# Performance work log

Measured on AMD Instinct MI355X. Metric: run time of the kernel, lower is better.

The kernel has to match this reference:

```python
import jax, jax.numpy as jnp
import numpy as np

NUM_HEADS = 12
MASK_BIAS = -1000.0


def setup_inputs() -> dict:
    key = jax.random.key(0)
    k1, k2, k3, k4 = jax.random.split(key, 4)
    B, N, C = 2, 2048, 768
    x = jax.random.normal(k1, (B, N, C), dtype=jnp.float32)
    # key-padding mask: 1.0 = masked-out position (gets -1000 bias), 0.0 = visible
    mask = jax.random.randint(k2, (B, N), 0, 2).astype(jnp.float32)
    qkv_w = jax.random.normal(k3, (3 * C, C), dtype=jnp.float32) * (1.0 / np.sqrt(C))
    proj_w = jax.random.normal(k4, (C, C), dtype=jnp.float32) * (1.0 / np.sqrt(C))
    proj_b = jnp.zeros((C,), dtype=jnp.float32)
    return {"x": x, "mask": mask, "qkv_w": qkv_w, "proj_w": proj_w, "proj_b": proj_b}


def reference(x, mask, qkv_w, proj_w, proj_b):
    B, N, C = x.shape
    H = NUM_HEADS
    D = C // H
    scale = D ** (-0.5)
    # qkv: Linear without bias -> [B, N, 3C] -> [3, B, H, N, D]
    qkv = (x @ qkv_w.T).reshape(B, N, 3, H, D).transpose(2, 0, 3, 1, 4)
    q, k, v = qkv[0], qkv[1], qkv[2]
    # scores [B, H, N, N]
    attn = jnp.einsum("bhqd,bhkd->bhqk", q, k) * scale
    attn = attn + mask[:, None, None, :] * MASK_BIAS
    attn = jax.nn.softmax(attn, axis=-1)
    out = jnp.einsum("bhqk,bhkd->bhqd", attn, v)  # [B, H, N, D]
    out = out.transpose(0, 2, 1, 3).reshape(B, N, C)
    return out @ proj_w.T + proj_b
```

## Files before the change

kernel.cpp:

```cpp
#include <hip/hip_runtime.h>

typedef __bf16 bf16_t;
typedef __bf16 bf16x8 __attribute__((ext_vector_type(8)));
typedef float f32x4 __attribute__((ext_vector_type(4)));

#define NUM_B 2
#define NUM_H 12
#define SEQ_N 2048
#define DIM_C 768
#define HEAD_D 64
#define BH_CNT (NUM_B * NUM_H)
#define MTOK (NUM_B * SEQ_N)
#define QSCALE 0.1803368801111137f

#define AS1(p) ((const __attribute__((address_space(1))) void*)(p))
#define AS3(p) ((__attribute__((address_space(3))) void*)(p))

__global__ __launch_bounds__(256) void cvt_scan_kernel(
    const float* __restrict__ s0, const float* __restrict__ s1,
    const float* __restrict__ s2, const float* __restrict__ msk,
    bf16_t* __restrict__ d0, bf16_t* __restrict__ d1, bf16_t* __restrict__ d2,
    int* __restrict__ src, bf16_t* __restrict__ wp, int* __restrict__ cnts,
    int nb0, int nb1, int nb2) {
  __shared__ int psum[256];
  const int blk = blockIdx.x;
  const int t = threadIdx.x;
  if (blk >= nb0 + nb1 + nb2) {
    const int b = blk - (nb0 + nb1 + nb2);
    const float* mb = msk + (size_t)b * SEQ_N;
    int vis[8], c = 0;
#pragma unroll
    for (int j = 0; j < 8; ++j) {
      vis[j] = (mb[t * 8 + j] == 0.0f) ? 1 : 0;
      c += vis[j];
    }
    psum[t] = c;
    __syncthreads();
    for (int off = 1; off < 256; off <<= 1) {
      int v = (t >= off) ? psum[t - off] : 0;
      __syncthreads();
      psum[t] += v;
      __syncthreads();
    }
    const int total = psum[255];
    int vpos = psum[t] - c;
    int mpos = total + (t * 8 - (psum[t] - c));
#pragma unroll
    for (int j = 0; j < 8; ++j) {
      const int tok = t * 8 + j;
      if (vis[j]) {
        src[b * SEQ_N + vpos] = b * SEQ_N + tok;
        wp[b * SEQ_N + vpos] = (bf16_t)1.0f;
        ++vpos;
      } else {
        src[b * SEQ_N + mpos] = b * SEQ_N + tok;
        wp[b * SEQ_N + mpos] = (bf16_t)0.0f;
        ++mpos;
      }
    }
    if (t == 0) {
      cnts[b * 2] = (total + 63) & ~63;
      cnts[b * 2 + 1] = total;
    }
    return;
  }
  const float* sp;
  bf16_t* dp;
  size_t off;
  if (blk < nb0) {
    sp = s0; dp = d0; off = (size_t)blk * 2048;
  } else if (blk < nb0 + nb1) {
    sp = s1; dp = d1; off = (size_t)(blk - nb0) * 2048;
  } else {
    sp = s2; dp = d2; off = (size_t)(blk - nb0 - nb1) * 2048;
  }
  const size_t i = off + (size_t)t * 8;
  float4 f0 = *reinterpret_cast<const float4*>(&sp[i]);
  float4 f1 = *reinterpret_cast<const float4*>(&sp[i + 4]);
  union { ushort4 u; bf16_t h[4]; } p0, p1;
  p0.h[0] = (bf16_t)f0.x; p0.h[1] = (bf16_t)f0.y;
  p0.h[2] = (bf16_t)f0.z; p0.h[3] = (bf16_t)f0.w;
  p1.h[0] = (bf16_t)f1.x; p1.h[1] = (bf16_t)f1.y;
  p1.h[2] = (bf16_t)f1.z; p1.h[3] = (bf16_t)f1.w;
  *reinterpret_cast<ushort4*>(&dp[i]) = p0.u;
  *reinterpret_cast<ushort4*>(&dp[i + 4]) = p1.u;
}

__global__ __launch_bounds__(256, 3) void gemm_qkv_kernel(
    const bf16_t* __restrict__ A, const bf16_t* __restrict__ W,
    const int* __restrict__ src, const int* __restrict__ cnts,
    bf16_t* __restrict__ out) {
  __shared__ __align__(16) bf16_t As[2][128 * 32];
  __shared__ __align__(16) bf16_t Bs[2][128 * 32];

  const int tid = threadIdx.x;
  const int wave = tid >> 6, lane = tid & 63;
  const int quad = lane >> 4, l16 = lane & 15;
  const int m0 = blockIdx.y * 128, n0 = blockIdx.x * 128;
  const int wm = (wave >> 1) * 64, wn = (wave & 1) * 64;
  const bool isQ = (n0 < DIM_C);

  if (!isQ) {
    const int b = m0 >> 11;
    if ((m0 & 2047) >= cnts[b * 2]) return;
  }

  f32x4 acc[4][4] = {};

  const int srow = tid >> 2;
  const int scol = ((tid & 3) ^ ((tid >> 3) & 3)) * 8;
  int ar0, ar1;
  if (isQ) {
    ar0 = m0 + srow;
    ar1 = m0 + srow + 64;
  } else {
    ar0 = src[m0 + srow];
    ar1 = src[m0 + srow + 64];
  }
  const bf16_t* gA0 = A + (size_t)ar0 * DIM_C + scol;
  const bf16_t* gA1 = A + (size_t)ar1 * DIM_C + scol;
  const bf16_t* gB0 = W + (size_t)(n0 + srow) * DIM_C + scol;
  const bf16_t* gB1 = W + (size_t)(n0 + srow + 64) * DIM_C + scol;
  const int lb = wave * 512;

  auto issue = [&](int buf, int k0) {
    __builtin_amdgcn_global_load_lds(AS1(gA0 + k0), AS3(&As[buf][lb]), 16, 0, 0);
    __builtin_amdgcn_global_load_lds(AS1(gA1 + k0), AS3(&As[buf][lb + 2048]), 16, 0, 0);
    __builtin_amdgcn_global_load_lds(AS1(gB0 + k0), AS3(&Bs[buf][lb]), 16, 0, 0);
    __builtin_amdgcn_global_load_lds(AS1(gB1 + k0), AS3(&Bs[buf][lb + 2048]), 16, 0, 0);
  };

  issue(0, 0);
  int cur = 0;
  const int sw = (l16 >> 1) & 3;
  for (int step = 0; step < DIM_C / 32; ++step) {
    __syncthreads();
    if (step + 1 < DIM_C / 32) issue(cur ^ 1, (step + 1) * 32);

    bf16x8 aF[4], bF[4];
#pragma unroll
    for (int mi = 0; mi < 4; ++mi)
      aF[mi] = *reinterpret_cast<const bf16x8*>(
          &As[cur][(wm + mi * 16 + l16) * 32 + ((quad ^ sw) * 8)]);
#pragma unroll
    for (int ni = 0; ni < 4; ++ni)
      bF[ni] = *reinterpret_cast<const bf16x8*>(
          &Bs[cur][(wn + ni * 16 + l16) * 32 + ((quad ^ sw) * 8)]);
#pragma unroll
    for (int mi = 0; mi < 4; ++mi)
#pragma unroll
      for (int ni = 0; ni < 4; ++ni)
        acc[mi][ni] = __builtin_amdgcn_mfma_f32_16x16x32_bf16(aF[mi], bF[ni],
                                                              acc[mi][ni], 0, 0, 0);
    cur ^= 1;
  }

  const size_t per = (size_t)BH_CNT * SEQ_N * HEAD_D;
#pragma unroll
  for (int mi = 0; mi < 4; ++mi) {
#pragma unroll
    for (int ni = 0; ni < 4; ++ni) {
      const int gmB = m0 + wm + mi * 16 + quad * 4;
      const int gn = n0 + wn + ni * 16 + l16;
      const int b = gmB >> 11;
      if (isQ) {
        const int h = gn >> 6, d = gn & 63;
#pragma unroll
        for (int r = 0; r < 4; ++r) {
          const int gm = gmB + r;
          const int tok = gm & 2047;
          out[(((size_t)((gm >> 11) * NUM_H + h) * SEQ_N + tok) * HEAD_D + d)] =
              (bf16_t)(acc[mi][ni][r] * QSCALE);
        }
      } else if (n0 < 2 * DIM_C) {
        const int rem = gn - DIM_C;
        const int h = rem >> 6, d = rem & 63;
#pragma unroll
        for (int r = 0; r < 4; ++r) {
          const int pos = (gmB + r) & 2047;
          out[per + (((size_t)(b * NUM_H + h) * SEQ_N + pos) * HEAD_D + d)] =
              (bf16_t)acc[mi][ni][r];
        }
      } else {
        const int rem = gn - 2 * DIM_C;
        const int h = rem >> 6, d = rem & 63;
        const int pos0 = gmB & 2047;
        const int count = cnts[b * 2 + 1];
        union { ushort4 u; bf16_t h4[4]; } pk;
#pragma unroll
        for (int r = 0; r < 4; ++r)
          pk.h4[r] = (pos0 + r < count) ? (bf16_t)acc[mi][ni][r] : (bf16_t)0.0f;
        *reinterpret_cast<ushort4*>(
            &out[2 * per + (((size_t)(b * NUM_H + h) * HEAD_D + d) * SEQ_N + pos0)]) =
            pk.u;
      }
    }
  }
}

__global__ __launch_bounds__(256, 3) void gemm_proj_kernel(
    const bf16_t* __restrict__ A, const bf16_t* __restrict__ W,
    const float* __restrict__ bias, float* __restrict__ out) {
  __shared__ __align__(16) bf16_t As[2][128 * 32];
  __shared__ __align__(16) bf16_t Bs[2][128 * 32];

  const int tid = threadIdx.x;
  const int wave = tid >> 6, lane = tid & 63;
  const int quad = lane >> 4, l16 = lane & 15;
  const int m0 = blockIdx.y * 128, n0 = blockIdx.x * 128;
  const int wm = (wave >> 1) * 64, wn = (wave & 1) * 64;

  f32x4 acc[4][4] = {};

  const int srow = tid >> 2;
  const int scol = ((tid & 3) ^ ((tid >> 3) & 3)) * 8;
  const bf16_t* gA0 = A + (size_t)(m0 + srow) * DIM_C + scol;
  const bf16_t* gA1 = A + (size_t)(m0 + srow + 64) * DIM_C + scol;
  const bf16_t* gB0 = W + (size_t)(n0 + srow) * DIM_C + scol;
  const bf16_t* gB1 = W + (size_t)(n0 + srow + 64) * DIM_C + scol;
  const int lb = wave * 512;

  auto issue = [&](int buf, int k0) {
    __builtin_amdgcn_global_load_lds(AS1(gA0 + k0), AS3(&As[buf][lb]), 16, 0, 0);
    __builtin_amdgcn_global_load_lds(AS1(gA1 + k0), AS3(&As[buf][lb + 2048]), 16, 0, 0);
    __builtin_amdgcn_global_load_lds(AS1(gB0 + k0), AS3(&Bs[buf][lb]), 16, 0, 0);
    __builtin_amdgcn_global_load_lds(AS1(gB1 + k0), AS3(&Bs[buf][lb + 2048]), 16, 0, 0);
  };

  issue(0, 0);
  int cur = 0;
  const int sw = (l16 >> 1) & 3;
  for (int step = 0; step < DIM_C / 32; ++step) {
    __syncthreads();
    if (step + 1 < DIM_C / 32) issue(cur ^ 1, (step + 1) * 32);

    bf16x8 aF[4], bF[4];
#pragma unroll
    for (int mi = 0; mi < 4; ++mi)
      aF[mi] = *reinterpret_cast<const bf16x8*>(
          &As[cur][(wm + mi * 16 + l16) * 32 + ((quad ^ sw) * 8)]);
#pragma unroll
    for (int ni = 0; ni < 4; ++ni)
      bF[ni] = *reinterpret_cast<const bf16x8*>(
          &Bs[cur][(wn + ni * 16 + l16) * 32 + ((quad ^ sw) * 8)]);
#pragma unroll
    for (int mi = 0; mi < 4; ++mi)
#pragma unroll
      for (int ni = 0; ni < 4; ++ni)
        acc[mi][ni] = __builtin_amdgcn_mfma_f32_16x16x32_bf16(aF[mi], bF[ni],
                                                              acc[mi][ni], 0, 0, 0);
    cur ^= 1;
  }

#pragma unroll
  for (int mi = 0; mi < 4; ++mi) {
#pragma unroll
    for (int ni = 0; ni < 4; ++ni) {
      const int gmB = m0 + wm + mi * 16 + quad * 4;
      const int gn = n0 + wn + ni * 16 + l16;
      const float bv = bias[gn];
#pragma unroll
      for (int r = 0; r < 4; ++r)
        out[(size_t)(gmB + r) * DIM_C + gn] = acc[mi][ni][r] + bv;
    }
  }
}

__global__ __launch_bounds__(256, 4) void attn_kernel(
    const bf16_t* __restrict__ q, const bf16_t* __restrict__ k,
    const bf16_t* __restrict__ vt, const bf16_t* __restrict__ wp,
    const int* __restrict__ cnts, bf16_t* __restrict__ ctx) {
  __shared__ __align__(16) bf16_t Ks[2][64 * 64];
  __shared__ __align__(16) bf16_t Vs[2][64 * 64];
  __shared__ __align__(16) bf16_t Ps[4][1024];

  const int tid = threadIdx.x;
  const int wave = tid >> 6, lane = tid & 63;
  const int quad = lane >> 4, l16 = lane & 15;
  const int bh = blockIdx.y;
  const int b = bh / NUM_H, h = bh - b * NUM_H;
  const int q0 = blockIdx.x * 64 + wave * 16;
  const int cntPad = cnts[b * 2];

  const bf16_t* qb = q + (size_t)bh * SEQ_N * HEAD_D;
  const bf16_t* kb = k + (size_t)bh * SEQ_N * HEAD_D;
  const bf16_t* vtb = vt + (size_t)bh * HEAD_D * SEQ_N;
  const bf16_t* wb = wp + (size_t)b * SEQ_N;

  bf16x8 qf[2];
#pragma unroll
  for (int ks = 0; ks < 2; ++ks)
    qf[ks] = *reinterpret_cast<const bf16x8*>(
        &qb[(size_t)(q0 + l16) * HEAD_D + ks * 32 + quad * 8]);

  f32x4 acc[4] = {};
  f32x4 acc_l = {};

  const int srow = tid >> 3;
  const int scol = ((tid & 7) ^ ((tid >> 3) & 7)) * 8;
  const bf16_t* gK0 = kb + (size_t)srow * HEAD_D + scol;
  const bf16_t* gK1 = kb + (size_t)(srow + 32) * HEAD_D + scol;
  const bf16_t* gV0 = vtb + (size_t)srow * SEQ_N + scol;
  const bf16_t* gV1 = vtb + (size_t)(srow + 32) * SEQ_N + scol;
  const int lb = wave * 512;

  auto issueKV = [&](int buf, int key0) {
    __builtin_amdgcn_global_load_lds(AS1(gK0 + (size_t)key0 * HEAD_D),
                                     AS3(&Ks[buf][lb]), 16, 0, 0);
    __builtin_amdgcn_global_load_lds(AS1(gK1 + (size_t)key0 * HEAD_D),
                                     AS3(&Ks[buf][lb + 2048]), 16, 0, 0);
    __builtin_amdgcn_global_load_lds(AS1(gV0 + key0), AS3(&Vs[buf][lb]), 16, 0, 0);
    __builtin_amdgcn_global_load_lds(AS1(gV1 + key0), AS3(&Vs[buf][lb + 2048]),
                                     16, 0, 0);
  };

  issueKV(0, 0);
  int cur = 0;
  const int swz = l16 & 7;
  const int psbase = wave * 1024 + l16 * 64;
  for (int key0 = 0; key0 < cntPad; key0 += 64) {
    __syncthreads();
    if (key0 + 64 < cntPad) issueKV(cur ^ 1, key0 + 64);

    f32x4 s[4];
#pragma unroll
    for (int kt = 0; kt < 4; ++kt) {
      const int row = kt * 16 + l16;
      bf16x8 kf0 = *reinterpret_cast<const bf16x8*>(
          &Ks[cur][row * 64 + ((quad ^ swz) * 8)]);
      bf16x8 kf1 = *reinterpret_cast<const bf16x8*>(
          &Ks[cur][row * 64 + (((4 + quad) ^ swz) * 8)]);
      f32x4 z = {0.0f, 0.0f, 0.0f, 0.0f};
      z = __builtin_amdgcn_mfma_f32_16x16x32_bf16(kf0, qf[0], z, 0, 0, 0);
      s[kt] = __builtin_amdgcn_mfma_f32_16x16x32_bf16(kf1, qf[1], z, 0, 0, 0);
    }

#pragma unroll
    for (int kt = 0; kt < 4; ++kt) {
      union { ushort4 u; bf16_t h4[4]; } pk;
      pk.h4[0] = (bf16_t)exp2f(s[kt][0]);
      pk.h4[1] = (bf16_t)exp2f(s[kt][1]);
      pk.h4[2] = (bf16_t)exp2f(s[kt][2]);
      pk.h4[3] = (bf16_t)exp2f(s[kt][3]);
      const int c = kt * 2 + (quad >> 1);
      *reinterpret_cast<ushort4*>(
          &Ps[0][psbase + ((c ^ swz) << 3) + ((quad & 1) << 2)]) = pk.u;
    }

    bf16x8 pf0 = *reinterpret_cast<const bf16x8*>(
        &Ps[0][psbase + ((quad ^ swz) << 3)]);
    bf16x8 pf1 = *reinterpret_cast<const bf16x8*>(
        &Ps[0][psbase + (((4 + quad) ^ swz) << 3)]);
    bf16x8 wf0 = *reinterpret_cast<const bf16x8*>(&wb[key0 + quad * 8]);
    bf16x8 wf1 = *reinterpret_cast<const bf16x8*>(&wb[key0 + 32 + quad * 8]);
    acc_l = __builtin_amdgcn_mfma_f32_16x16x32_bf16(pf0, wf0, acc_l, 0, 0, 0);
    acc_l = __builtin_amdgcn_mfma_f32_16x16x32_bf16(pf1, wf1, acc_l, 0, 0, 0);

#pragma unroll
    for (int dt = 0; dt < 4; ++dt) {
      const int row = dt * 16 + l16;
      bf16x8 vf0 = *reinterpret_cast<const bf16x8*>(
          &Vs[cur][row * 64 + ((quad ^ swz) * 8)]);
      bf16x8 vf1 = *reinterpret_cast<const bf16x8*>(
          &Vs[cur][row * 64 + (((4 + quad) ^ swz) * 8)]);
      acc[dt] = __builtin_amdgcn_mfma_f32_16x16x32_bf16(pf0, vf0, acc[dt], 0, 0, 0);
      acc[dt] = __builtin_amdgcn_mfma_f32_16x16x32_bf16(pf1, vf1, acc[dt], 0, 0, 0);
    }
    cur ^= 1;
  }

  float rl[4];
#pragma unroll
  for (int r = 0; r < 4; ++r) rl[r] = 1.0f / acc_l[r];
#pragma unroll
  for (int dt = 0; dt < 4; ++dt)
#pragma unroll
    for (int r = 0; r < 4; ++r) {
      const int tok = q0 + quad * 4 + r;
      ctx[((size_t)b * SEQ_N + tok) * DIM_C + h * HEAD_D + dt * 16 + l16] =
          (bf16_t)(acc[dt][r] * rl[r]);
    }
}

extern "C" void kernel_launch(void* const* d_in, const int* in_sizes, int n_in,
                              void* d_out, int out_size, void* d_ws,
                              size_t ws_size, hipStream_t stream) {
  const float* x = (const float*)d_in[0];
  const float* mask = (const float*)d_in[1];
  const float* qkv_w = (const float*)d_in[2];
  const float* proj_w = (const float*)d_in[3];
  const float* proj_b = (const float*)d_in[4];
  float* out = (float*)d_out;

  const size_t nx = (size_t)MTOK * DIM_C;
  const size_t nqw = (size_t)3 * DIM_C * DIM_C;
  const size_t npw = (size_t)DIM_C * DIM_C;
  const size_t per = (size_t)BH_CNT * SEQ_N * HEAD_D;

  bf16_t* xb = (bf16_t*)d_ws;
  bf16_t* qwb = xb + nx;
  bf16_t* pwb = qwb + nqw;
  bf16_t* wpb = pwb + npw;
  int* srcb = (int*)(wpb + MTOK);
  int* cntsb = srcb + MTOK;
  bf16_t* qkv = (bf16_t*)(cntsb + 8);
  bf16_t* ctx = qkv + 3 * per;

  const int nb0 = (int)(nx / 2048), nb1 = (int)(nqw / 2048),
            nb2 = (int)(npw / 2048);

  cvt_scan_kernel<<<nb0 + nb1 + nb2 + NUM_B, 256, 0, stream>>>(
      x, qkv_w, proj_w, mask, xb, qwb, pwb, srcb, wpb, cntsb, nb0, nb1, nb2);
  gemm_qkv_kernel<<<dim3(3 * DIM_C / 128, MTOK / 128), 256, 0, stream>>>(
      xb, qwb, srcb, cntsb, qkv);
  attn_kernel<<<dim3(SEQ_N / 64, BH_CNT), 256, 0, stream>>>(
      qkv, qkv + per, qkv + 2 * per, wpb, cntsb, ctx);
  gemm_proj_kernel<<<dim3(DIM_C / 128, MTOK / 128), 256, 0, stream>>>(
      ctx, pwb, proj_b, out);
}
```

Measured before the change: 150.5 us.

## Stage only K in LDS with 128-key tiles, read V directly from global

The attention loop now double-buffers only K in shared memory and uses 128-key tiles, split into two 64-key halves per barrier. V fragments are loaded straight from global memory into registers for each half. This halves the number of barriers and frees LDS that V staging used to occupy. In exchange, V loads are no longer prefetched through LDS and may expose global latency; the occupancy hint also drops from 4 to 3 blocks.

```diff
diff --git a/kernel.cpp b/kernel.cpp
--- a/kernel.cpp
+++ b/kernel.cpp
@@ -266,12 +266,11 @@
   }
 }
 
-__global__ __launch_bounds__(256, 4) void attn_kernel(
+__global__ __launch_bounds__(256, 3) void attn_kernel(
     const bf16_t* __restrict__ q, const bf16_t* __restrict__ k,
     const bf16_t* __restrict__ vt, const bf16_t* __restrict__ wp,
     const int* __restrict__ cnts, bf16_t* __restrict__ ctx) {
-  __shared__ __align__(16) bf16_t Ks[2][64 * 64];
-  __shared__ __align__(16) bf16_t Vs[2][64 * 64];
+  __shared__ __align__(16) bf16_t Ks[2][128 * 64];
   __shared__ __align__(16) bf16_t Ps[4][1024];
 
   const int tid = threadIdx.x;
@@ -297,74 +296,81 @@
   f32x4 acc_l = {};
 
   const int srow = tid >> 3;
-  const int scol = ((tid & 7) ^ ((tid >> 3) & 7)) * 8;
-  const bf16_t* gK0 = kb + (size_t)srow * HEAD_D + scol;
-  const bf16_t* gK1 = kb + (size_t)(srow + 32) * HEAD_D + scol;
-  const bf16_t* gV0 = vtb + (size_t)srow * SEQ_N + scol;
-  const bf16_t* gV1 = vtb + (size_t)(srow + 32) * SEQ_N + scol;
+  const int scol = ((tid & 7) ^ (srow & 7)) * 8;
+  const bf16_t* gK = kb + (size_t)srow * HEAD_D + scol;
   const int lb = wave * 512;
 
-  auto issueKV = [&](int buf, int key0) {
-    __builtin_amdgcn_global_load_lds(AS1(gK0 + (size_t)key0 * HEAD_D),
-                                     AS3(&Ks[buf][lb]), 16, 0, 0);
-    __builtin_amdgcn_global_load_lds(AS1(gK1 + (size_t)key0 * HEAD_D),
-                                     AS3(&Ks[buf][lb + 2048]), 16, 0, 0);
-    __builtin_amdgcn_global_load_lds(AS1(gV0 + key0), AS3(&Vs[buf][lb]), 16, 0, 0);
-    __builtin_amdgcn_global_load_lds(AS1(gV1 + key0), AS3(&Vs[buf][lb + 2048]),
-                                     16, 0, 0);
+  auto issueK = [&](int buf, int key0) {
+#pragma unroll
+    for (int p = 0; p < 4; ++p)
+      __builtin_amdgcn_global_load_lds(
+          AS1(gK + (size_t)(key0 + p * 32) * HEAD_D),
+          AS3(&Ks[buf][p * 2048 + lb]), 16, 0, 0);
   };
 
-  issueKV(0, 0);
+  issueK(0, 0);
   int cur = 0;
   const int swz = l16 & 7;
   const int psbase = wave * 1024 + l16 * 64;
-  for (int key0 = 0; key0 < cntPad; key0 += 64) {
+
+  for (int key0 = 0; key0 < cntPad; key0 += 128) {
     __syncthreads();
-    if (key0 + 64 < cntPad) issueKV(cur ^ 1, key0 + 64);
-
-    f32x4 s[4];
-#pragma unroll
-    for (int kt = 0; kt < 4; ++kt) {
-      const int row = kt * 16 + l16;
-      bf16x8 kf0 = *reinterpret_cast<const bf16x8*>(
-          &Ks[cur][row * 64 + ((quad ^ swz) * 8)]);
-      bf16x8 kf1 = *reinterpret_cast<const bf16x8*>(
-          &Ks[cur][row * 64 + (((4 + quad) ^ swz) * 8)]);
-      f32x4 z = {0.0f, 0.0f, 0.0f, 0.0f};
-      z = __builtin_amdgcn_mfma_f32_16x16x32_bf16(kf0, qf[0], z, 0, 0, 0);
-      s[kt] = __builtin_amdgcn_mfma_f32_16x16x32_bf16(kf1, qf[1], z, 0, 0, 0);
-    }
-
-#pragma unroll
-    for (int kt = 0; kt < 4; ++kt) {
-      union { ushort4 u; bf16_t h4[4]; } pk;
-      pk.h4[0] = (bf16_t)exp2f(s[kt][0]);
-      pk.h4[1] = (bf16_t)exp2f(s[kt][1]);
-      pk.h4[2] = (bf16_t)exp2f(s[kt][2]);
-      pk.h4[3] = (bf16_t)exp2f(s[kt][3]);
-      const int c = kt * 2 + (quad >> 1);
-      *reinterpret_cast<ushort4*>(
-          &Ps[0][psbase + ((c ^ swz) << 3) + ((quad & 1) << 2)]) = pk.u;
-    }
-
-    bf16x8 pf0 = *reinterpret_cast<const bf16x8*>(
-        &Ps[0][psbase + ((quad ^ swz) << 3)]);
-    bf16x8 pf1 = *reinterpret_cast<const bf16x8*>(
-        &Ps[0][psbase + (((4 + quad) ^ swz) << 3)]);
-    bf16x8 wf0 = *reinterpret_cast<const bf16x8*>(&wb[key0 + quad * 8]);
-    bf16x8 wf1 = *reinterpret_cast<const bf16x8*>(&wb[key0 + 32 + quad * 8]);
-    acc_l = __builtin_amdgcn_mfma_f32_16x16x32_bf16(pf0, wf0, acc_l, 0, 0, 0);
-    acc_l = __builtin_amdgcn_mfma_f32_16x16x32_bf16(pf1, wf1, acc_l, 0, 0, 0);
-
-#pragma unroll
-    for (int dt = 0; dt < 4; ++dt) {
-      const int row = dt * 16 + l16;
-      bf16x8 vf0 = *reinterpret_cast<const bf16x8*>(
-          &Vs[cur][row * 64 + ((quad ^ swz) * 8)]);
-      bf16x8 vf1 = *reinterpret_cast<const bf16x8*>(
-          &Vs[cur][row * 64 + (((4 + quad) ^ swz) * 8)]);
-      acc[dt] = __builtin_amdgcn_mfma_f32_16x16x32_bf16(pf0, vf0, acc[dt], 0, 0, 0);
-      acc[dt] = __builtin_amdgcn_mfma_f32_16x16x32_bf16(pf1, vf1, acc[dt], 0, 0, 0);
+    if (key0 + 128 < cntPad) issueK(cur ^ 1, key0 + 128);
+
+#pragma unroll
+    for (int hf = 0; hf < 2; ++hf) {
+      const int kbase = key0 + hf * 64;
+      if (kbase >= cntPad) break;
+
+      bf16x8 vf[4][2];
+#pragma unroll
+      for (int dt = 0; dt < 4; ++dt) {
+        const bf16_t* vr = &vtb[(size_t)(dt * 16 + l16) * SEQ_N + kbase];
+        vf[dt][0] = *reinterpret_cast<const bf16x8*>(&vr[quad * 8]);
+        vf[dt][1] = *reinterpret_cast<const bf16x8*>(&vr[32 + quad * 8]);
+      }
+
+      f32x4 s[4];
+#pragma unroll
+      for (int kt = 0; kt < 4; ++kt) {
+        const int row = hf * 64 + kt * 16 + l16;
+        bf16x8 kf0 = *reinterpret_cast<const bf16x8*>(
+            &Ks[cur][row * 64 + ((quad ^ swz) * 8)]);
+        bf16x8 kf1 = *reinterpret_cast<const bf16x8*>(
+            &Ks[cur][row * 64 + (((4 + quad) ^ swz) * 8)]);
+        f32x4 z = {0.0f, 0.0f, 0.0f, 0.0f};
+        z = __builtin_amdgcn_mfma_f32_16x16x32_bf16(kf0, qf[0], z, 0, 0, 0);
+        s[kt] = __builtin_amdgcn_mfma_f32_16x16x32_bf16(kf1, qf[1], z, 0, 0, 0);
+      }
+
+#pragma unroll
+      for (int kt = 0; kt < 4; ++kt) {
+        union { ushort4 u; bf16_t h4[4]; } pk;
+        pk.h4[0] = (bf16_t)exp2f(s[kt][0]);
+        pk.h4[1] = (bf16_t)exp2f(s[kt][1]);
+        pk.h4[2] = (bf16_t)exp2f(s[kt][2]);
+        pk.h4[3] = (bf16_t)exp2f(s[kt][3]);
+        const int c = kt * 2 + (quad >> 1);
+        *reinterpret_cast<ushort4*>(
+            &Ps[0][psbase + ((c ^ swz) << 3) + ((quad & 1) << 2)]) = pk.u;
+      }
+
+      bf16x8 pf0 = *reinterpret_cast<const bf16x8*>(
+          &Ps[0][psbase + ((quad ^ swz) << 3)]);
+      bf16x8 pf1 = *reinterpret_cast<const bf16x8*>(
+          &Ps[0][psbase + (((4 + quad) ^ swz) << 3)]);
+      bf16x8 wf0 = *reinterpret_cast<const bf16x8*>(&wb[kbase + quad * 8]);
+      bf16x8 wf1 = *reinterpret_cast<const bf16x8*>(&wb[kbase + 32 + quad * 8]);
+      acc_l = __builtin_amdgcn_mfma_f32_16x16x32_bf16(pf0, wf0, acc_l, 0, 0, 0);
+      acc_l = __builtin_amdgcn_mfma_f32_16x16x32_bf16(pf1, wf1, acc_l, 0, 0, 0);
+
+#pragma unroll
+      for (int dt = 0; dt < 4; ++dt) {
+        acc[dt] =
+            __builtin_amdgcn_mfma_f32_16x16x32_bf16(pf0, vf[dt][0], acc[dt], 0, 0, 0);
+        acc[dt] =
+            __builtin_amdgcn_mfma_f32_16x16x32_bf16(pf1, vf[dt][1], acc[dt], 0, 0, 0);
+      }
     }
     cur ^= 1;
   }
```

Result: slower. 175.6 us (+16.7%).
